# Kernel tuning notes

Hardware: AMD Instinct MI355X
Metric: run time of the kernel (lower is better)

Reference implementation:

```python
import jax, jax.numpy as jnp
import numpy as np


def setup_inputs() -> dict:
    key = jax.random.key(0)
    ks = jax.random.split(key, 8)
    B, T, D, E = 16, 1024, 1024, 64
    s = lambda fan: 1.0 / np.sqrt(fan)
    return {
        "seq": jax.random.normal(ks[0], (B, T, D), jnp.float32),
        "pi": jax.random.uniform(ks[1], (E,), jnp.float32),
        "beta_raw": jnp.full((D,), 2.1972246, jnp.float32),  # logit(0.9)
        "p1_w": jax.random.normal(ks[2], (4 * D, 2 * D), jnp.float32) * s(2 * D),
        "p1_b": jnp.zeros((4 * D,), jnp.float32),
        "p2_w": jax.random.normal(ks[3], (D, 4 * D), jnp.float32) * s(4 * D),
        "p2_b": jnp.zeros((D,), jnp.float32),
        "W_w": jax.random.normal(ks[4], (E, D), jnp.float32) * s(D),
        "W_b": jnp.zeros((E,), jnp.float32),
    }


def reference(seq, pi, beta_raw, p1_w, p1_b, p2_w, p2_b, W_w, W_b):
    B, T, D = seq.shape
    beta = jax.nn.sigmoid(beta_raw)  # (D,), per-channel EMA coefficient
    x = jnp.transpose(seq[:, : T - 1, :], (1, 0, 2))  # (T-1, B, D), steps 0..T-2

    # Sequential EMA recurrence h_t = beta*h_{t-1} + x_t (h_{-1}=0)
    def step(h, x_t):
        h = beta * h + x_t
        return h, h

    _, hs = jax.lax.scan(step, jnp.zeros((B, D), seq.dtype), x)  # (T-1, B, D)

    # Predictor MLP over all timesteps at once (use_beta + use_ant branch)
    inp = jnp.concatenate([x, hs], axis=-1)  # (T-1, B, 2D)
    hid = jax.nn.relu(jnp.einsum('tbi,hi->tbh', inp, p1_w) + p1_b)  # (T-1, B, 4D)
    x_hat = jnp.einsum('tbh,dh->tbd', hid, p2_w) + p2_b  # (T-1, B, D)

    # Linear router + pi scaling
    logits = (jnp.einsum('tbd,ed->tbe', x_hat, W_w) + W_b) * pi  # (T-1, B, E)
    return logits, x_hat
```

## Files before the change

kernel.cpp:

```cpp
#include <hip/hip_runtime.h>
#include <hip/hip_bf16.h>
#include <cstdint>
#include <cstddef>

using bf16 = __hip_bfloat16;
typedef __bf16 bf16x8 __attribute__((ext_vector_type(8)));
typedef float f32x4 __attribute__((ext_vector_type(4)));
typedef float f32x16 __attribute__((ext_vector_type(16)));

#define BB 16
#define TT 1024
#define DD 1024
#define EE 64
#define MREAL 16368
#define MPAD  16384
#define NCHUNK 16
#define CHUNK 64

__device__ __forceinline__ void gload_lds16(const void* g, void* l) {
  __builtin_amdgcn_global_load_lds((const __attribute__((address_space(1))) void*)g,
                                   (__attribute__((address_space(3))) void*)l,
                                   16, 0, 0);
}

__device__ __forceinline__ float sigmoidf_(float x) {
  return 1.0f / (1.0f + __expf(-x));
}

__global__ void f2b(const float* __restrict__ src, bf16* __restrict__ dst, int n) {
  int i = (blockIdx.x * blockDim.x + threadIdx.x) * 8;
  if (i < n) {
    float4 v0 = *reinterpret_cast<const float4*>(src + i);
    float4 v1 = *reinterpret_cast<const float4*>(src + i + 4);
    alignas(16) bf16 tmp[8];
    tmp[0] = __float2bfloat16(v0.x); tmp[1] = __float2bfloat16(v0.y);
    tmp[2] = __float2bfloat16(v0.z); tmp[3] = __float2bfloat16(v0.w);
    tmp[4] = __float2bfloat16(v1.x); tmp[5] = __float2bfloat16(v1.y);
    tmp[6] = __float2bfloat16(v1.z); tmp[7] = __float2bfloat16(v1.w);
    *reinterpret_cast<float4*>(dst + i) = *reinterpret_cast<const float4*>(tmp);
  }
}

__global__ void ema_ends(const float* __restrict__ seq, const float* __restrict__ beta_raw,
                         float* __restrict__ ends) {
  int tid = blockIdx.x * blockDim.x + threadIdx.x;
  int d = tid & (DD - 1);
  int b = (tid >> 10) & (BB - 1);
  int c = tid >> 14;
  float beta = sigmoidf_(beta_raw[d]);
  int t0 = c * CHUNK;
  int len = min(CHUNK, (TT - 1) - t0);
  const float* p = seq + (size_t)b * TT * DD + (size_t)t0 * DD + d;
  float h = 0.0f;
#pragma unroll 8
  for (int j = 0; j < len; ++j) h = fmaf(beta, h, p[(size_t)j * DD]);
  ends[tid] = h;
}

__global__ void ema_carry(const float* __restrict__ ends, const float* __restrict__ beta_raw,
                          float* __restrict__ carry) {
  int tid = blockIdx.x * blockDim.x + threadIdx.x;
  int d = tid & (DD - 1);
  float beta = sigmoidf_(beta_raw[d]);
  float bl = beta;
  bl *= bl; bl *= bl; bl *= bl; bl *= bl; bl *= bl; bl *= bl;
  float run = 0.0f;
#pragma unroll
  for (int c = 0; c < NCHUNK; ++c) {
    carry[c * (BB * DD) + tid] = run;
    run = ends[c * (BB * DD) + tid] + bl * run;
  }
}

__global__ void ema_write(const float* __restrict__ seq, const float* __restrict__ beta_raw,
                          const float* __restrict__ carry, bf16* __restrict__ A) {
  int tid = blockIdx.x * blockDim.x + threadIdx.x;
  int d = tid & (DD - 1);
  int b = (tid >> 10) & (BB - 1);
  int c = tid >> 14;
  float beta = sigmoidf_(beta_raw[d]);
  int t0 = c * CHUNK;
  int len = min(CHUNK, (TT - 1) - t0);
  const float* p = seq + (size_t)b * TT * DD + (size_t)t0 * DD + d;
  float h = carry[tid];
#pragma unroll 4
  for (int j = 0; j < len; ++j) {
    float x = p[(size_t)j * DD];
    h = fmaf(beta, h, x);
    size_t m = (size_t)(t0 + j) * BB + b;
    A[m * (2 * DD) + d]      = __float2bfloat16(x);
    A[m * (2 * DD) + DD + d] = __float2bfloat16(h);
  }
}

template <bool RELU, bool DUAL_OUT>
__global__ __launch_bounds__(256, 2)
void gemm_bt(const bf16* __restrict__ A, const bf16* __restrict__ B,
             const float* __restrict__ bias, bf16* __restrict__ outb,
             float* __restrict__ outf, int N, int K) {
  __shared__ alignas(16) bf16 As[128 * 64];
  __shared__ alignas(16) bf16 Bs[256 * 64];
  const int tid  = threadIdx.x;
  const int wave = tid >> 6;
  const int lane = tid & 63;
  const int bm = blockIdx.y * 128;
  const int bn = blockIdx.x * 256;

  const int srow8 = lane >> 3;
  const int scg   = (lane & 7) ^ srow8;
  const bf16* gA = A + (size_t)(bm + wave * 32 + srow8) * K + scg * 8;
  const bf16* gB = B + (size_t)(bn + wave * 64 + srow8) * K + scg * 8;
  bf16* lA = &As[(wave * 32 + srow8) * 64 + (lane & 7) * 8];
  bf16* lB = &Bs[(wave * 64 + srow8) * 64 + (lane & 7) * 8];

  const int lr   = lane & 31;
  const int half = lane >> 5;
  const int wm = (wave >> 1) * 64;
  const int wn = (wave & 1) * 128;
  int aoff[2], boff[4];
#pragma unroll
  for (int i = 0; i < 2; ++i) aoff[i] = (wm + i * 32 + lr) * 64;
#pragma unroll
  for (int j = 0; j < 4; ++j) boff[j] = (wn + j * 32 + lr) * 64;
  int swz[4];
#pragma unroll
  for (int kk = 0; kk < 4; ++kk) swz[kk] = ((kk * 2 + half) ^ (lr & 7)) * 8;

  f32x16 acc[2][4] = {};

  for (int k0 = 0; k0 < K; k0 += 64) {
    __syncthreads();
#pragma unroll
    for (int t = 0; t < 4; ++t)
      gload_lds16(gA + (size_t)t * 8 * K + k0, lA + t * 8 * 64);
#pragma unroll
    for (int t = 0; t < 8; ++t)
      gload_lds16(gB + (size_t)t * 8 * K + k0, lB + t * 8 * 64);
    __syncthreads();
#pragma unroll
    for (int kk = 0; kk < 4; ++kk) {
      bf16x8 a0 = *reinterpret_cast<const bf16x8*>(&As[aoff[0] + swz[kk]]);
      bf16x8 a1 = *reinterpret_cast<const bf16x8*>(&As[aoff[1] + swz[kk]]);
      bf16x8 b0 = *reinterpret_cast<const bf16x8*>(&Bs[boff[0] + swz[kk]]);
      bf16x8 b1 = *reinterpret_cast<const bf16x8*>(&Bs[boff[1] + swz[kk]]);
      bf16x8 b2 = *reinterpret_cast<const bf16x8*>(&Bs[boff[2] + swz[kk]]);
      bf16x8 b3 = *reinterpret_cast<const bf16x8*>(&Bs[boff[3] + swz[kk]]);
      acc[0][0] = __builtin_amdgcn_mfma_f32_32x32x16_bf16(a0, b0, acc[0][0], 0, 0, 0);
      acc[0][1] = __builtin_amdgcn_mfma_f32_32x32x16_bf16(a0, b1, acc[0][1], 0, 0, 0);
      acc[0][2] = __builtin_amdgcn_mfma_f32_32x32x16_bf16(a0, b2, acc[0][2], 0, 0, 0);
      acc[0][3] = __builtin_amdgcn_mfma_f32_32x32x16_bf16(a0, b3, acc[0][3], 0, 0, 0);
      acc[1][0] = __builtin_amdgcn_mfma_f32_32x32x16_bf16(a1, b0, acc[1][0], 0, 0, 0);
      acc[1][1] = __builtin_amdgcn_mfma_f32_32x32x16_bf16(a1, b1, acc[1][1], 0, 0, 0);
      acc[1][2] = __builtin_amdgcn_mfma_f32_32x32x16_bf16(a1, b2, acc[1][2], 0, 0, 0);
      acc[1][3] = __builtin_amdgcn_mfma_f32_32x32x16_bf16(a1, b3, acc[1][3], 0, 0, 0);
    }
  }

#pragma unroll
  for (int i = 0; i < 2; ++i) {
#pragma unroll
    for (int j = 0; j < 4; ++j) {
      const int n = bn + wn + j * 32 + lr;
      const float bv = bias[n];
#pragma unroll
      for (int r = 0; r < 16; ++r) {
        const int m = bm + wm + i * 32 + (r & 3) + 8 * (r >> 2) + 4 * half;
        float v = acc[i][j][r] + bv;
        if (RELU) v = fmaxf(v, 0.0f);
        outb[(size_t)m * N + n] = __float2bfloat16(v);
        if (DUAL_OUT) {
          if (m < MREAL) outf[(size_t)m * N + n] = v;
        }
      }
    }
  }
}

__global__ __launch_bounds__(256)
void gemm_router(const bf16* __restrict__ A, const bf16* __restrict__ B,
                 const float* __restrict__ Wb, const float* __restrict__ pi,
                 float* __restrict__ out) {
  const int K = DD;
  __shared__ alignas(16) bf16 As[64 * 32];
  __shared__ alignas(16) bf16 Bs[64 * 32];
  const int tid  = threadIdx.x;
  const int wave = tid >> 6;
  const int lane = tid & 63;
  const int bm = blockIdx.x * 64;
  const int srow = wave * 16 + (lane >> 2);
  const int scol = (lane & 3) * 8;
  const bf16* gA = A + (size_t)(bm + srow) * K + scol;
  const bf16* gB = B + (size_t)srow * K + scol;
  bf16* lA = &As[srow * 32 + scol];
  bf16* lB = &Bs[srow * 32 + scol];
  const int lr = lane & 15;
  const int quad = lane >> 4;
  f32x4 acc[4] = {};
  for (int k0 = 0; k0 < K; k0 += 32) {
    __syncthreads();
    gload_lds16(gA + k0, lA);
    gload_lds16(gB + k0, lB);
    __syncthreads();
    bf16x8 af = *reinterpret_cast<const bf16x8*>(&As[(wave * 16 + lr) * 32 + quad * 8]);
#pragma unroll
    for (int j = 0; j < 4; ++j) {
      bf16x8 bf_ = *reinterpret_cast<const bf16x8*>(&Bs[(j * 16 + lr) * 32 + quad * 8]);
      acc[j] = __builtin_amdgcn_mfma_f32_16x16x32_bf16(af, bf_, acc[j], 0, 0, 0);
    }
  }
#pragma unroll
  for (int j = 0; j < 4; ++j) {
    const int e = j * 16 + lr;
    const float wb = Wb[e], pv = pi[e];
#pragma unroll
    for (int r = 0; r < 4; ++r) {
      const int m = bm + wave * 16 + quad * 4 + r;
      if (m < MREAL) out[(size_t)m * EE + e] = (acc[j][r] + wb) * pv;
    }
  }
}

extern "C" void kernel_launch(void* const* d_in, const int* in_sizes, int n_in,
                              void* d_out, int out_size, void* d_ws, size_t ws_size,
                              hipStream_t stream) {
  const float* seq      = (const float*)d_in[0];
  const float* pi       = (const float*)d_in[1];
  const float* beta_raw = (const float*)d_in[2];
  const float* p1_w     = (const float*)d_in[3];
  const float* p1_b     = (const float*)d_in[4];
  const float* p2_w     = (const float*)d_in[5];
  const float* p2_b     = (const float*)d_in[6];
  const float* W_w      = (const float*)d_in[7];
  const float* W_b      = (const float*)d_in[8];

  constexpr size_t A_off    = 0;
  constexpr size_t A_sz     = (size_t)MPAD * 2 * DD * sizeof(bf16);
  constexpr size_t W1_off   = A_off + A_sz;
  constexpr size_t W1_sz    = (size_t)4 * DD * 2 * DD * sizeof(bf16);
  constexpr size_t HID_off  = W1_off + W1_sz;
  constexpr size_t HID_sz   = (size_t)MPAD * 4 * DD * sizeof(bf16);
  constexpr size_t W2_off   = HID_off + HID_sz;
  constexpr size_t W2_sz    = (size_t)DD * 4 * DD * sizeof(bf16);
  constexpr size_t W3_off   = W2_off + W2_sz;
  constexpr size_t W3_sz    = (size_t)EE * DD * sizeof(bf16);
  constexpr size_t ENDS_off = W3_off + W3_sz;
  constexpr size_t ENDS_sz  = (size_t)NCHUNK * BB * DD * sizeof(float);
  constexpr size_t CARRY_off = ENDS_off + ENDS_sz;

  char* ws = (char*)d_ws;
  bf16*  Abuf = (bf16*)(ws + A_off);
  bf16*  W1   = (bf16*)(ws + W1_off);
  bf16*  HID  = (bf16*)(ws + HID_off);
  bf16*  W2   = (bf16*)(ws + W2_off);
  bf16*  W3   = (bf16*)(ws + W3_off);
  float* ENDS = (float*)(ws + ENDS_off);
  float* CARRY = (float*)(ws + CARRY_off);
  bf16*  XH   = (bf16*)(ws + A_off);

  float* out_logits = (float*)d_out;
  float* out_xhat   = out_logits + (size_t)MREAL * EE;

  f2b<<<(4 * DD * 2 * DD / 8 + 255) / 256, 256, 0, stream>>>(p1_w, W1, 4 * DD * 2 * DD);
  f2b<<<(DD * 4 * DD / 8 + 255) / 256, 256, 0, stream>>>(p2_w, W2, DD * 4 * DD);
  f2b<<<(EE * DD / 8 + 255) / 256, 256, 0, stream>>>(W_w, W3, EE * DD);

  ema_ends<<<NCHUNK * BB * DD / 256, 256, 0, stream>>>(seq, beta_raw, ENDS);
  ema_carry<<<BB * DD / 256, 256, 0, stream>>>(ENDS, beta_raw, CARRY);
  ema_write<<<NCHUNK * BB * DD / 256, 256, 0, stream>>>(seq, beta_raw, CARRY, Abuf);
  (void)hipMemsetAsync(ws + A_off + (size_t)MREAL * 2 * DD * sizeof(bf16), 0,
                       (size_t)(MPAD - MREAL) * 2 * DD * sizeof(bf16), stream);

  gemm_bt<true, false><<<dim3(4 * DD / 256, MPAD / 128), 256, 0, stream>>>(
      Abuf, W1, p1_b, HID, nullptr, 4 * DD, 2 * DD);

  gemm_bt<false, true><<<dim3(DD / 256, MPAD / 128), 256, 0, stream>>>(
      HID, W2, p2_b, XH, out_xhat, DD, 4 * DD);

  gemm_router<<<MPAD / 64, 256, 0, stream>>>(XH, W3, W_b, pi, out_logits);
}
```

Measured before the change: 644.7 us.

## Replace GEMM with 256x256 8-wave double-buffered pipelined MFMA kernel

Result: faster. 574.3 us (-10.9%).

```diff
diff --git a/kernel.cpp b/kernel.cpp
--- a/kernel.cpp
+++ b/kernel.cpp
@@ -6,7 +6,6 @@
 using bf16 = __hip_bfloat16;
 typedef __bf16 bf16x8 __attribute__((ext_vector_type(8)));
 typedef float f32x4 __attribute__((ext_vector_type(4)));
-typedef float f32x16 __attribute__((ext_vector_type(16)));
 
 #define BB 16
 #define TT 1024
@@ -93,80 +92,156 @@
   }
 }
 
+
+#define RD_A(d, fb)                                                          \
+  _Pragma("unroll")                                                          \
+  for (int f = 0; f < 4; ++f)                                                \
+    _Pragma("unroll")                                                        \
+    for (int s = 0; s < 2; ++s)                                              \
+      a[f][s] = *reinterpret_cast<const bf16x8*>(                            \
+          &lds[(d) * 32768 + ArdB + ((fb) + f) * 1024 + roff[s]]);
+
+#define RD_B(d, j0)                                                          \
+  _Pragma("unroll")                                                          \
+  for (int jj = 0; jj < 2; ++jj)                                             \
+    _Pragma("unroll")                                                        \
+    for (int s = 0; s < 2; ++s)                                              \
+      b[(j0) + jj][s] = *reinterpret_cast<const bf16x8*>(                    \
+          &lds[(d) * 32768 + BrdB + ((j0) + jj) * 1024 + roff[s]]);
+
+#define STAGE_A(d, h, kq)                                                    \
+  {                                                                          \
+    _Pragma("unroll")                                                        \
+    for (int t = 0; t < 2; ++t)                                              \
+      gload_lds16(gA + ((size_t)((h) * 128 + t * 8) * K + (kq) * 64),        \
+                  &lds[(d) * 32768 + (h) * 8192 + stbase + t * 512]);        \
+  }
+
+#define STAGE_B(d, h, kq)                                                    \
+  {                                                                          \
+    _Pragma("unroll")                                                        \
+    for (int t = 0; t < 2; ++t)                                              \
+      gload_lds16(gB + ((size_t)((h) * 128 + t * 8) * K + (kq) * 64),        \
+                  &lds[(d) * 32768 + 16384 + (h) * 8192 + stbase + t * 512]); \
+  }
+
+#define MFMA_Q(fb, j0)                                                       \
+  _Pragma("unroll")                                                          \
+  for (int s = 0; s < 2; ++s)                                                \
+    _Pragma("unroll")                                                        \
+    for (int f = 0; f < 4; ++f)                                              \
+      _Pragma("unroll")                                                      \
+      for (int j = 0; j < 2; ++j)                                            \
+        acc[(fb) + f][(j0) + j] = __builtin_amdgcn_mfma_f32_16x16x32_bf16(   \
+            a[f][s], b[(j0) + j][s], acc[(fb) + f][(j0) + j], 0, 0, 0);
+
+#define PH_MID()                                                             \
+  __builtin_amdgcn_s_barrier();                                              \
+  asm volatile("s_waitcnt lgkmcnt(0)" ::: "memory");                         \
+  __builtin_amdgcn_sched_barrier(0);                                         \
+  __builtin_amdgcn_s_setprio(1);
+
+#define PH_END()                                                             \
+  __builtin_amdgcn_s_setprio(0);                                             \
+  __builtin_amdgcn_sched_barrier(0);                                         \
+  __builtin_amdgcn_s_barrier();
+
+#define KTILE(d)                                                             \
+  {                                                                          \
+    const int kA = (q + 1 < NT) ? (q + 1) : (NT - 1);                        \
+    const int kB = (q + 2 < NT) ? (q + 2) : (NT - 1);                        \
+                                                   \
+    RD_A(d, 0);                                                              \
+    RD_B(d, 0);                                                              \
+    STAGE_A((d) ^ 1, 0, kA);                                                 \
+    asm volatile("s_waitcnt lgkmcnt(8)" ::: "memory");                       \
+    PH_MID(); MFMA_Q(0, 0); PH_END();                                        \
+                                                   \
+    RD_B(d, 2);                                                              \
+    STAGE_A((d) ^ 1, 1, kA);                                                 \
+    PH_MID(); MFMA_Q(0, 2); PH_END();                                        \
+                                                   \
+    RD_A(d, 4);                                                              \
+    STAGE_B((d), 0, kB);                                                     \
+    PH_MID(); MFMA_Q(4, 2); PH_END();                                        \
+                                                   \
+    STAGE_B((d), 1, kB);                                                     \
+    asm volatile("s_waitcnt vmcnt(4)" ::: "memory");                         \
+    PH_MID(); MFMA_Q(4, 0); PH_END();                                        \
+    ++q;                                                                     \
+  }
+
 template <bool RELU, bool DUAL_OUT>
-__global__ __launch_bounds__(256, 2)
-void gemm_bt(const bf16* __restrict__ A, const bf16* __restrict__ B,
-             const float* __restrict__ bias, bf16* __restrict__ outb,
-             float* __restrict__ outf, int N, int K) {
-  __shared__ alignas(16) bf16 As[128 * 64];
-  __shared__ alignas(16) bf16 Bs[256 * 64];
+__global__ __launch_bounds__(512, 2)
+void gemm8(const bf16* __restrict__ A, const bf16* __restrict__ B,
+           const float* __restrict__ bias, bf16* __restrict__ outb,
+           float* __restrict__ outf, int N, int K) {
+  __shared__ bf16 lds[65536];
   const int tid  = threadIdx.x;
   const int wave = tid >> 6;
   const int lane = tid & 63;
-  const int bm = blockIdx.y * 128;
-  const int bn = blockIdx.x * 256;
-
-  const int srow8 = lane >> 3;
-  const int scg   = (lane & 7) ^ srow8;
-  const bf16* gA = A + (size_t)(bm + wave * 32 + srow8) * K + scg * 8;
-  const bf16* gB = B + (size_t)(bn + wave * 64 + srow8) * K + scg * 8;
-  bf16* lA = &As[(wave * 32 + srow8) * 64 + (lane & 7) * 8];
-  bf16* lB = &Bs[(wave * 64 + srow8) * 64 + (lane & 7) * 8];
-
-  const int lr   = lane & 31;
-  const int half = lane >> 5;
-  const int wm = (wave >> 1) * 64;
-  const int wn = (wave & 1) * 128;
-  int aoff[2], boff[4];
-#pragma unroll
-  for (int i = 0; i < 2; ++i) aoff[i] = (wm + i * 32 + lr) * 64;
-#pragma unroll
-  for (int j = 0; j < 4; ++j) boff[j] = (wn + j * 32 + lr) * 64;
-  int swz[4];
-#pragma unroll
-  for (int kk = 0; kk < 4; ++kk) swz[kk] = ((kk * 2 + half) ^ (lr & 7)) * 8;
-
-  f32x16 acc[2][4] = {};
-
-  for (int k0 = 0; k0 < K; k0 += 64) {
-    __syncthreads();
-#pragma unroll
-    for (int t = 0; t < 4; ++t)
-      gload_lds16(gA + (size_t)t * 8 * K + k0, lA + t * 8 * 64);
-#pragma unroll
-    for (int t = 0; t < 8; ++t)
-      gload_lds16(gB + (size_t)t * 8 * K + k0, lB + t * 8 * 64);
-    __syncthreads();
-#pragma unroll
-    for (int kk = 0; kk < 4; ++kk) {
-      bf16x8 a0 = *reinterpret_cast<const bf16x8*>(&As[aoff[0] + swz[kk]]);
-      bf16x8 a1 = *reinterpret_cast<const bf16x8*>(&As[aoff[1] + swz[kk]]);
-      bf16x8 b0 = *reinterpret_cast<const bf16x8*>(&Bs[boff[0] + swz[kk]]);
-      bf16x8 b1 = *reinterpret_cast<const bf16x8*>(&Bs[boff[1] + swz[kk]]);
-      bf16x8 b2 = *reinterpret_cast<const bf16x8*>(&Bs[boff[2] + swz[kk]]);
-      bf16x8 b3 = *reinterpret_cast<const bf16x8*>(&Bs[boff[3] + swz[kk]]);
-      acc[0][0] = __builtin_amdgcn_mfma_f32_32x32x16_bf16(a0, b0, acc[0][0], 0, 0, 0);
-      acc[0][1] = __builtin_amdgcn_mfma_f32_32x32x16_bf16(a0, b1, acc[0][1], 0, 0, 0);
-      acc[0][2] = __builtin_amdgcn_mfma_f32_32x32x16_bf16(a0, b2, acc[0][2], 0, 0, 0);
-      acc[0][3] = __builtin_amdgcn_mfma_f32_32x32x16_bf16(a0, b3, acc[0][3], 0, 0, 0);
-      acc[1][0] = __builtin_amdgcn_mfma_f32_32x32x16_bf16(a1, b0, acc[1][0], 0, 0, 0);
-      acc[1][1] = __builtin_amdgcn_mfma_f32_32x32x16_bf16(a1, b1, acc[1][1], 0, 0, 0);
-      acc[1][2] = __builtin_amdgcn_mfma_f32_32x32x16_bf16(a1, b2, acc[1][2], 0, 0, 0);
-      acc[1][3] = __builtin_amdgcn_mfma_f32_32x32x16_bf16(a1, b3, acc[1][3], 0, 0, 0);
-    }
-  }
-
-#pragma unroll
-  for (int i = 0; i < 2; ++i) {
+  const int wm = wave >> 2;
+  const int wn = wave & 3;
+
+  const int gx   = gridDim.x;
+  const int nwg  = gx * gridDim.y;
+  const int orig = blockIdx.y * gx + blockIdx.x;
+  const int swz  = (orig & 7) * (nwg >> 3) + (orig >> 3);
+  const int bm = (swz / gx) * 256;
+  const int bn = (swz % gx) * 256;
+
+  const int srow = lane >> 3;
+  const int scg  = (lane & 7) ^ srow;
+  const bf16* gA = A + (size_t)(bm + wave * 16 + srow) * K + scg * 8;
+  const bf16* gB = B + (size_t)(bn + wave * 16 + srow) * K + scg * 8;
+  const int stbase = wave * 1024;
+
+  int roff[2];
+#pragma unroll
+  for (int s = 0; s < 2; ++s)
+    roff[s] = (lane & 15) * 64 + (((s * 4 + (lane >> 4)) ^ (lane & 7)) * 8);
+  const int ArdB = wm * 8192;
+  const int BrdB = 16384 + (wn >> 1) * 8192 + (wn & 1) * 4096;
+
+  f32x4 acc[8][4] = {};
+  bf16x8 a[4][2], b[4][2];
+  const int NT = K >> 6;
+  int q = 0;
+
+  STAGE_A(0, 0, 0);
+  STAGE_A(0, 1, 0);
+  STAGE_B(0, 0, 0);
+  STAGE_B(0, 1, 0);
+  STAGE_B(1, 0, 1);
+  STAGE_B(1, 1, 1);
+  asm volatile("s_waitcnt vmcnt(4)" ::: "memory");
+  __builtin_amdgcn_s_barrier();
+
+#pragma unroll 1
+  for (int it = 0; it < (NT >> 1); ++it) {
+    KTILE(0);
+    KTILE(1);
+  }
+  asm volatile("s_waitcnt vmcnt(0)" ::: "memory");
+
+  float bv[4];
+  int   ncol[4];
+#pragma unroll
+  for (int j = 0; j < 4; ++j) {
+    ncol[j] = bn + wn * 64 + j * 16 + (lane & 15);
+    bv[j]   = bias[ncol[j]];
+  }
+#pragma unroll
+  for (int f = 0; f < 8; ++f) {
+    const int m0 = bm + wm * 128 + f * 16 + (lane >> 4) * 4;
 #pragma unroll
     for (int j = 0; j < 4; ++j) {
-      const int n = bn + wn + j * 32 + lr;
-      const float bv = bias[n];
-#pragma unroll
-      for (int r = 0; r < 16; ++r) {
-        const int m = bm + wm + i * 32 + (r & 3) + 8 * (r >> 2) + 4 * half;
-        float v = acc[i][j][r] + bv;
+      const int n = ncol[j];
+#pragma unroll
+      for (int r = 0; r < 4; ++r) {
+        float v = acc[f][j][r] + bv[j];
         if (RELU) v = fmaxf(v, 0.0f);
+        const int m = m0 + r;
         outb[(size_t)m * N + n] = __float2bfloat16(v);
         if (DUAL_OUT) {
           if (m < MREAL) outf[(size_t)m * N + n] = v;
@@ -270,10 +345,10 @@
   (void)hipMemsetAsync(ws + A_off + (size_t)MREAL * 2 * DD * sizeof(bf16), 0,
                        (size_t)(MPAD - MREAL) * 2 * DD * sizeof(bf16), stream);
 
-  gemm_bt<true, false><<<dim3(4 * DD / 256, MPAD / 128), 256, 0, stream>>>(
+  gemm8<true, false><<<dim3(4 * DD / 256, MPAD / 256), 512, 0, stream>>>(
       Abuf, W1, p1_b, HID, nullptr, 4 * DD, 2 * DD);
 
-  gemm_bt<false, true><<<dim3(DD / 256, MPAD / 128), 256, 0, stream>>>(
+  gemm8<false, true><<<dim3(DD / 256, MPAD / 256), 512, 0, stream>>>(
       HID, W2, p2_b, XH, out_xhat, DD, 4 * DD);
 
   gemm_router<<<MPAD / 64, 256, 0, stream>>>(XH, W3, W_b, pi, out_logits);
```
